# Kernel tuning notes

Hardware: AMD Instinct MI355X
Metric: run time of the kernel (lower is better)

## Reference

```python
import jax, jax.numpy as jnp
import numpy as np

B, N, L, VALID_Y = 1, 3072, 256, 200
DIM_X, DIM_Y, H = 3072, 1536, 24
HD = DIM_X // H  # 128
EPS_MOD, EPS_RMS = 1e-6, 1e-5


def _mod_rmsnorm(t, scale):
    # F.rms_norm (no weight) then modulate by (1 + scale)
    tn = t * jax.lax.rsqrt(jnp.mean(t * t, axis=-1, keepdims=True) + EPS_MOD)
    return tn * (1.0 + scale[:, None, :])


def _rmsnorm(t, w):
    return t * jax.lax.rsqrt(jnp.mean(t * t, axis=-1, keepdims=True) + EPS_RMS) * w


def _rope(t, cos, sin):
    # t: (B, N, H, HD); cos/sin: (N, H, HD/2); even/odd interleaved rotary
    te, to = t[..., 0::2], t[..., 1::2]
    cp = te * cos - to * sin
    sp = te * sin + to * cos
    return jnp.stack([cp, sp], axis=-1).reshape(t.shape)


def setup_inputs() -> dict:
    key = jax.random.key(0)
    ks = jax.random.split(key, 12)
    s = 0.02
    d = {}
    d['x'] = jax.random.normal(ks[0], (B, N, DIM_X), jnp.float32)
    d['y'] = jax.random.normal(ks[1], (B, L, DIM_Y), jnp.float32)
    d['scale_x'] = jax.random.normal(ks[2], (B, DIM_X), jnp.float32) * 0.1
    d['scale_y'] = jax.random.normal(ks[3], (B, DIM_Y), jnp.float32) * 0.1
    ang = jax.random.uniform(ks[4], (N, H, HD // 2), jnp.float32, 0.0, 2.0 * np.pi)
    d['rope_cos'] = jnp.cos(ang)
    d['rope_sin'] = jnp.sin(ang)
    d['W_qkv_x'] = jax.random.normal(ks[5], (DIM_X, 3 * DIM_X), jnp.float32) * s
    d['b_qkv_x'] = jnp.zeros((3 * DIM_X,), jnp.float32)
    d['W_qkv_y'] = jax.random.normal(ks[6], (DIM_Y, 3 * DIM_X), jnp.float32) * s
    d['b_qkv_y'] = jnp.zeros((3 * DIM_X,), jnp.float32)
    d['w_qn_x'] = jnp.ones((HD,), jnp.float32)
    d['w_kn_x'] = jnp.ones((HD,), jnp.float32)
    d['w_qn_y'] = jnp.ones((HD,), jnp.float32)
    d['w_kn_y'] = jnp.ones((HD,), jnp.float32)
    d['W_proj_x'] = jax.random.normal(ks[7], (DIM_X, DIM_X), jnp.float32) * s
    d['b_proj_x'] = jnp.zeros((DIM_X,), jnp.float32)
    d['W_proj_y'] = jax.random.normal(ks[8], (DIM_X, DIM_Y), jnp.float32) * s
    d['b_proj_y'] = jnp.zeros((DIM_Y,), jnp.float32)
    # B=1 packing: all N video tokens + first VALID_Y text tokens of flattened (N+L)
    d['valid_token_indices'] = jnp.arange(N + VALID_Y, dtype=jnp.int32)
    return d


def reference(x, y, scale_x, scale_y, rope_cos, rope_sin,
              W_qkv_x, b_qkv_x, W_qkv_y, b_qkv_y,
              w_qn_x, w_kn_x, w_qn_y, w_kn_y,
              W_proj_x, b_proj_x, W_proj_y, b_proj_y,
              valid_token_indices):
    # ---- visual stream: modulated RMSNorm -> qkv -> qk-norm -> RoPE ----
    xm = _mod_rmsnorm(x, scale_x)
    qkv_x = (xm @ W_qkv_x + b_qkv_x).reshape(B, N, 3, H, HD)
    qkv_x = jnp.transpose(qkv_x, (2, 0, 1, 3, 4))  # (3,B,N,H,HD)
    q_x, k_x, v_x = qkv_x[0], qkv_x[1], qkv_x[2]
    q_x = _rope(_rmsnorm(q_x, w_qn_x), rope_cos, rope_sin)
    k_x = _rope(_rmsnorm(k_x, w_kn_x), rope_cos, rope_sin)
    # ---- text stream: modulated RMSNorm -> qkv -> qk-norm ----
    ym = _mod_rmsnorm(y, scale_y)
    qkv_y = (ym @ W_qkv_y + b_qkv_y).reshape(B, L, 3, H, HD)
    q_y, k_y, v_y = qkv_y[:, :, 0], qkv_y[:, :, 1], qkv_y[:, :, 2]
    q_y = _rmsnorm(q_y, w_qn_y)
    k_y = _rmsnorm(k_y, w_kn_y)
    # ---- unify_streams: concat, pack, gather valid tokens ----
    qkv = jnp.stack([
        jnp.concatenate([q_x, q_y], axis=1),
        jnp.concatenate([k_x, k_y], axis=1),
        jnp.concatenate([v_x, v_y], axis=1),
    ], axis=2).reshape(B * (N + L), 3, H, HD)
    qkv = qkv[valid_token_indices]  # (total, 3, H, HD)
    q, k, v = qkv[:, 0], qkv[:, 1], qkv[:, 2]
    # ---- varlen attention (B=1 -> single segment, full attention) ----
    scale = 1.0 / np.sqrt(HD)
    scores = jnp.einsum('qhd,khd->hqk', q, k) * scale
    attn = jax.nn.softmax(scores, axis=-1)
    out = jnp.einsum('hqk,khd->qhd', attn, v).reshape(-1, H * HD)  # (total, DIM_X)
    # ---- pad_and_split_xy: scatter back to padded stream, split ----
    padded = jnp.zeros((B * (N + L), H * HD), out.dtype).at[valid_token_indices].set(out)
    padded = padded.reshape(B, N + L, H * HD)
    x_out = padded[:, :N] @ W_proj_x + b_proj_x
    y_out = padded[:, N:] @ W_proj_y + b_proj_y
    return (x_out, y_out)
```

## Files before the change

kernel.cpp:

```cpp
#include <hip/hip_runtime.h>


typedef short short8 __attribute__((ext_vector_type(8)));
typedef float f32x4 __attribute__((ext_vector_type(4)));
typedef unsigned short ushort4v __attribute__((ext_vector_type(4)));

#define MFMA_BF16(a,b,c) __builtin_amdgcn_mfma_f32_16x16x32_bf16((a),(b),(c),0,0,0)

#define NH 24
#define SPAD 3328
#define SVAL 3272

__device__ __forceinline__ unsigned short bf16_rne(float f){
  unsigned int u = __builtin_bit_cast(unsigned int, f);
  u += 0x7FFFu + ((u >> 16) & 1u);
  return (unsigned short)(u >> 16);
}
__device__ __forceinline__ float bf2f(unsigned short h){
  unsigned int u = ((unsigned int)h) << 16;
  return __builtin_bit_cast(float, u);
}
__device__ __forceinline__ void gload16(const void* g, void* l){
  __builtin_amdgcn_global_load_lds(
      (const __attribute__((address_space(1))) unsigned int*)g,
      (__attribute__((address_space(3))) unsigned int*)l, 16, 0, 0);
}

__global__ __launch_bounds__(256) void transpose_w(
    const float* __restrict__ W, unsigned short* __restrict__ Wt, int K, int N)
{
  __shared__ unsigned short t[64][66];
  int n0 = blockIdx.x*64, k0 = blockIdx.y*64;
  int tid = threadIdx.x;
  int kr = tid >> 4, nc = (tid & 15) * 4;
  #pragma unroll
  for (int pass=0; pass<4; pass++){
    int k = kr + pass*16;
    float4 v = *(const float4*)(W + (size_t)(k0+k)*N + n0 + nc);
    ushort4v o;
    o.x = bf16_rne(v.x); o.y = bf16_rne(v.y);
    o.z = bf16_rne(v.z); o.w = bf16_rne(v.w);
    *(ushort4v*)&t[k][nc] = o;
  }
  __syncthreads();
  int nr = tid >> 3, kc = (tid & 7) * 8;
  #pragma unroll
  for (int pass=0; pass<2; pass++){
    int n = nr + pass*32;
    unsigned short buf[8];
    #pragma unroll
    for (int j=0;j<8;j++) buf[j] = t[kc+j][n];
    *(short8*)(Wt + (size_t)(n0+n)*K + k0 + kc) = *(short8*)&buf[0];
  }
}

template<int D>
__global__ __launch_bounds__(256) void modnorm(
    const float* __restrict__ X, const float* __restrict__ scale,
    unsigned short* __restrict__ out)
{
  int row = blockIdx.x;
  const float4* xv = (const float4*)(X + (size_t)row*D);
  float ss = 0.f;
  for (int i = threadIdx.x; i < D/4; i += 256){
    float4 v = xv[i];
    ss += v.x*v.x + v.y*v.y + v.z*v.z + v.w*v.w;
  }
  #pragma unroll
  for (int d=1; d<64; d<<=1) ss += __shfl_xor(ss, d);
  __shared__ float wsum[4];
  if ((threadIdx.x & 63) == 0) wsum[threadIdx.x >> 6] = ss;
  __syncthreads();
  float tot = wsum[0] + wsum[1] + wsum[2] + wsum[3];
  float rn = rsqrtf(tot*(1.0f/(float)D) + 1e-6f);
  const float4* sv = (const float4*)scale;
  for (int i = threadIdx.x; i < D/4; i += 256){
    float4 v = xv[i]; float4 s4 = sv[i];
    ushort4v o;
    o.x = bf16_rne(v.x*rn*(1.f+s4.x));
    o.y = bf16_rne(v.y*rn*(1.f+s4.y));
    o.z = bf16_rne(v.z*rn*(1.f+s4.z));
    o.w = bf16_rne(v.w*rn*(1.f+s4.w));
    *(ushort4v*)(out + (size_t)row*D + i*4) = o;
  }
}

template<typename CT, bool BIAS>
__global__ __launch_bounds__(256, 3) void gemm_bt(
    const unsigned short* __restrict__ A, const unsigned short* __restrict__ BT,
    const float* __restrict__ bias, CT* __restrict__ C,
    int M, int N, int K, int ldc, int klen)
{
  __shared__ unsigned short lA[128*32];
  __shared__ unsigned short lB[128*32];
  int tid = threadIdx.x, wave = tid>>6, lane = tid&63;
  int l16 = lane&15, g = lane>>4;
  int wr = wave>>1, wc = wave&1;

  int nwg = gridDim.x*gridDim.y;
  int orig = blockIdx.y*gridDim.x + blockIdx.x;
  int neo = orig;
  if ((nwg & 7) == 0){
    int q8 = nwg >> 3;
    neo = (orig & 7)*q8 + (orig >> 3);
  }
  int bx = neo / gridDim.y;
  int by = neo % gridDim.y;
  int bm = by*128, bn = bx*128;
  int kof = blockIdx.z * klen;
  CT* Cp = C + (size_t)blockIdx.z * M * (size_t)ldc;

  f32x4 acc[4][4] = {};

  for (int k0 = kof; k0 < kof + klen; k0 += 32){
    #pragma unroll
    for (int i=0;i<2;i++){
      int off = i*4096 + wave*1024 + lane*16;
      int row = off>>6;
      int sp  = (off>>4)&3;
      int sk  = (sp ^ (row&3))*8;
      gload16(A + (size_t)(bm+row)*K + k0 + sk, (char*)lA + i*4096 + wave*1024);
    }
    #pragma unroll
    for (int i=0;i<2;i++){
      int off = i*4096 + wave*1024 + lane*16;
      int row = off>>6;
      int sp  = (off>>4)&3;
      int sk  = (sp ^ (row&3))*8;
      gload16(BT + (size_t)(bn+row)*K + k0 + sk, (char*)lB + i*4096 + wave*1024);
    }
    __syncthreads();

    short8 a[4], b[4];
    #pragma unroll
    for (int m=0;m<4;m++){
      int row = wr*64 + m*16 + l16;
      int slot = g ^ (row&3);
      a[m] = *(const short8*)((const char*)lA + row*64 + slot*16);
    }
    #pragma unroll
    for (int n=0;n<4;n++){
      int row = wc*64 + n*16 + l16;
      int slot = g ^ (row&3);
      b[n] = *(const short8*)((const char*)lB + row*64 + slot*16);
    }
    __builtin_amdgcn_s_setprio(1);
    #pragma unroll
    for (int m=0;m<4;m++)
      #pragma unroll
      for (int n=0;n<4;n++)
        acc[m][n] = MFMA_BF16(a[m], b[n], acc[m][n]);
    __builtin_amdgcn_s_setprio(0);
    __syncthreads();
  }

  #pragma unroll
  for (int n=0;n<4;n++){
    int col = bn + wc*64 + n*16 + l16;
    float bv = BIAS ? bias[col] : 0.f;
    #pragma unroll
    for (int m=0;m<4;m++){
      int row0 = bm + wr*64 + m*16 + g*4;
      #pragma unroll
      for (int r=0;r<4;r++){
        float v = acc[m][n][r] + bv;
        if constexpr (sizeof(CT) == 4) Cp[(size_t)(row0+r)*ldc + col] = v;
        else                           Cp[(size_t)(row0+r)*ldc + col] = bf16_rne(v);
      }
    }
  }
}

__global__ __launch_bounds__(512, 2) void gemm_8ph(
    const unsigned short* __restrict__ A, const unsigned short* __restrict__ BT,
    const float* __restrict__ bias, unsigned short* __restrict__ C,
    int M, int N, int K, int ldc)
{
  __shared__ unsigned short lds[8][8192];

  int tid = threadIdx.x, wave = tid>>6, lane = tid&63;
  int l16 = lane&15, g = lane>>4;
  int wr = wave>>2, wc = wave&3;

  int nwg = gridDim.x*gridDim.y;
  int orig = blockIdx.y*gridDim.x + blockIdx.x;
  int neo = orig;
  if ((nwg & 7) == 0) neo = (orig & 7)*(nwg>>3) + (orig>>3);
  int bx = neo / gridDim.y, by = neo % gridDim.y;
  int bm = by*256, bn = bx*256;

  const int NT = K >> 6;

  auto STAGE = [&](int t, int op, int half, int b){
    int tc = t < NT ? t : NT-1;
    const unsigned short* src = op ? BT : A;
    int base_row = (op ? bn : bm) + half*128;
    int k0 = tc << 6;
    #pragma unroll
    for (int j=0;j<2;j++){
      int o = (j*8 + wave)*1024 + lane*16;
      int row = o>>7, slot = (o>>4)&7;
      int sk = (slot ^ (row&7))*8;
      gload16(src + (size_t)(base_row+row)*K + k0 + sk,
              (char*)&lds[(b<<2)|(op<<1)|half][0] + (j*8+wave)*1024);
    }
  };

  short8 afr[4], bfr[8];
  auto LDA = [&](int b, int p){
    const char* basep = (const char*)&lds[(b<<2)|wr][0];
    #pragma unroll
    for (int mm=0;mm<2;mm++){
      int row = (p*2+mm)*16 + l16;
      #pragma unroll
      for (int kk=0;kk<2;kk++)
        afr[mm*2+kk] = *(const short8*)(basep + row*128 + (((kk*4+g) ^ (row&7))<<4));
    }
  };
  auto LDB = [&](int b){
    const char* basep = (const char*)&lds[(b<<2)|2|(wc>>1)][0];
    int rbase = (wc&1)*64;
    #pragma unroll
    for (int n=0;n<4;n++){
      int row = rbase + n*16 + l16;
      #pragma unroll
      for (int kk=0;kk<2;kk++)
        bfr[n*2+kk] = *(const short8*)(basep + row*128 + (((kk*4+g) ^ (row&7))<<4));
    }
  };

  f32x4 acc[8][4] = {};

  STAGE(0,1,0,0); STAGE(0,1,1,0); STAGE(0,0,0,0); STAGE(0,0,1,0);
  STAGE(1,1,0,1); STAGE(1,1,1,1); STAGE(1,0,0,1);
  asm volatile("s_waitcnt vmcnt(6)" ::: "memory");
  __builtin_amdgcn_s_barrier();

  int NIT = NT >> 1;
  for (int i=0;i<NIT;i++){
    int T = 2*i;
    #pragma unroll
    for (int p=0;p<4;p++){
      if (p==0) LDB(0);
      LDA(0, p);
      if (p==0)      STAGE(T+1,0,1,1);
      else if (p==1) STAGE(T+2,1,0,0);
      else if (p==2) STAGE(T+2,1,1,0);
      else           STAGE(T+2,0,0,0);
      if (p==0) asm volatile("s_waitcnt lgkmcnt(8)" ::: "memory");
      __builtin_amdgcn_s_barrier();
      asm volatile("s_waitcnt lgkmcnt(0)" ::: "memory");
      __builtin_amdgcn_sched_barrier(0);
      __builtin_amdgcn_s_setprio(1);
      #pragma unroll
      for (int mm=0;mm<2;mm++)
        #pragma unroll
        for (int n=0;n<4;n++)
          #pragma unroll
          for (int kk=0;kk<2;kk++)
            acc[p*2+mm][n] = MFMA_BF16(afr[mm*2+kk], bfr[n*2+kk], acc[p*2+mm][n]);
      __builtin_amdgcn_s_setprio(0);
      if (p==3) asm volatile("s_waitcnt vmcnt(6)" ::: "memory");
      __builtin_amdgcn_s_barrier();
    }
    #pragma unroll
    for (int p=0;p<4;p++){
      if (p==0) LDB(1);
      LDA(1, p);
      if (p==0)      STAGE(T+2,0,1,0);
      else if (p==1) STAGE(T+3,1,0,1);
      else if (p==2) STAGE(T+3,1,1,1);
      else           STAGE(T+3,0,0,1);
      if (p==0) asm volatile("s_waitcnt lgkmcnt(8)" ::: "memory");
      __builtin_amdgcn_s_barrier();
      asm volatile("s_waitcnt lgkmcnt(0)" ::: "memory");
      __builtin_amdgcn_sched_barrier(0);
      __builtin_amdgcn_s_setprio(1);
      #pragma unroll
      for (int mm=0;mm<2;mm++)
        #pragma unroll
        for (int n=0;n<4;n++)
          #pragma unroll
          for (int kk=0;kk<2;kk++)
            acc[p*2+mm][n] = MFMA_BF16(afr[mm*2+kk], bfr[n*2+kk], acc[p*2+mm][n]);
      __builtin_amdgcn_s_setprio(0);
      if (p==3) asm volatile("s_waitcnt vmcnt(6)" ::: "memory");
      __builtin_amdgcn_s_barrier();
    }
  }

  #pragma unroll
  for (int n=0;n<4;n++){
    int col = bn + wc*64 + n*16 + l16;
    float bv = bias[col];
    #pragma unroll
    for (int m=0;m<8;m++){
      int row0 = bm + wr*128 + m*16 + g*4;
      #pragma unroll
      for (int r=0;r<4;r++)
        C[(size_t)(row0+r)*ldc + col] = bf16_rne(acc[m][n][r] + bv);
    }
  }
}

__global__ __launch_bounds__(256) void reduce2_bias_bf16(
    const float* __restrict__ part, const float* __restrict__ bias,
    unsigned short* __restrict__ out, int N, size_t tot)
{
  size_t idx = ((size_t)blockIdx.x*256 + threadIdx.x)*4;
  if (idx >= tot) return;
  float4 a = *(const float4*)(part + idx);
  float4 b = *(const float4*)(part + tot + idx);
  int col = (int)(idx % N);
  float4 bv = *(const float4*)(bias + col);
  ushort4v o;
  o.x = bf16_rne(a.x+b.x+bv.x);
  o.y = bf16_rne(a.y+b.y+bv.y);
  o.z = bf16_rne(a.z+b.z+bv.z);
  o.w = bf16_rne(a.w+b.w+bv.w);
  *(ushort4v*)(out + idx) = o;
}

__global__ __launch_bounds__(256) void reduce8_bias_f32(
    const float* __restrict__ part, const float* __restrict__ bias,
    float* __restrict__ out, int N, size_t tot)
{
  size_t idx = ((size_t)blockIdx.x*256 + threadIdx.x)*4;
  if (idx >= tot) return;
  int col = (int)(idx % N);
  float4 s = *(const float4*)(bias + col);
  #pragma unroll
  for (int c=0;c<8;c++){
    float4 a = *(const float4*)(part + (size_t)c*tot + idx);
    s.x += a.x; s.y += a.y; s.z += a.z; s.w += a.w;
  }
  *(float4*)(out + idx) = s;
}

__global__ __launch_bounds__(256) void fixup_qk(
    const unsigned short* __restrict__ QKV,
    const float* __restrict__ cosT, const float* __restrict__ sinT,
    const float* __restrict__ wqx, const float* __restrict__ wkx,
    const float* __restrict__ wqy, const float* __restrict__ wky,
    unsigned short* __restrict__ Qo, unsigned short* __restrict__ Ko)
{
  int wave = threadIdx.x >> 6, lane = threadIdx.x & 63;
  int bid = blockIdx.x*4 + wave;
  int t = bid / NH, h = bid % NH;
  bool isx = (t < 3072);

  const unsigned short* base = QKV + (size_t)t*9216 + h*128;
  unsigned int qraw = *(const unsigned int*)(base + 2*lane);
  unsigned int kraw = *(const unsigned int*)(base + 3072 + 2*lane);
  float q0 = bf2f((unsigned short)(qraw & 0xffff)), q1 = bf2f((unsigned short)(qraw >> 16));
  float k0 = bf2f((unsigned short)(kraw & 0xffff)), k1 = bf2f((unsigned short)(kraw >> 16));

  float sq = q0*q0 + q1*q1, sk = k0*k0 + k1*k1;
  #pragma unroll
  for (int d=1; d<64; d<<=1){ sq += __shfl_xor(sq, d); sk += __shfl_xor(sk, d); }
  float rq = rsqrtf(sq*(1.0f/128.0f) + 1e-5f);
  float rk = rsqrtf(sk*(1.0f/128.0f) + 1e-5f);

  const float* wq = isx ? wqx : wqy;
  const float* wk = isx ? wkx : wky;
  float a0 = q0*rq*wq[2*lane], a1 = q1*rq*wq[2*lane+1];
  float b0 = k0*rk*wk[2*lane], b1 = k1*rk*wk[2*lane+1];

  if (isx){
    size_t ci = ((size_t)t*NH + h)*64 + lane;
    float c = cosT[ci], s = sinT[ci];
    float t0 = a0*c - a1*s, t1 = a0*s + a1*c; a0 = t0; a1 = t1;
    t0 = b0*c - b1*s; t1 = b0*s + b1*c; b0 = t0; b1 = t1;
  }
  size_t oi = ((size_t)h*SPAD + t)*128 + 2*lane;
  *(unsigned int*)(Qo + oi) = (unsigned int)bf16_rne(a0) | ((unsigned int)bf16_rne(a1) << 16);
  *(unsigned int*)(Ko + oi) = (unsigned int)bf16_rne(b0) | ((unsigned int)bf16_rne(b1) << 16);
}

__global__ __launch_bounds__(256) void v_transpose(
    const unsigned short* __restrict__ QKV, unsigned short* __restrict__ VT)
{
  __shared__ unsigned short t[64][136];
  int h = blockIdx.x;
  int t0 = blockIdx.y*64;
  int tid = threadIdx.x;
  #pragma unroll
  for (int it=0; it<4; it++){
    int chunk = it*256 + tid;
    int r = chunk >> 4, c = chunk & 15;
    short8 v = *(const short8*)(QKV + (size_t)(t0 + r)*9216 + 6144 + h*128 + c*8);
    *(short8*)&t[r][c*8] = v;
  }
  __syncthreads();
  int d = tid >> 1, half = tid & 1;
  size_t ob = (size_t)(h*128 + d)*SPAD + t0 + half*32;
  #pragma unroll
  for (int j=0;j<32;j+=2){
    unsigned int v = (unsigned int)t[half*32 + j][d] | ((unsigned int)t[half*32 + j + 1][d] << 16);
    *(unsigned int*)(VT + ob + j) = v;
  }
}

__global__ __launch_bounds__(256, 3) void attn_fwd(
    const unsigned short* __restrict__ Q, const unsigned short* __restrict__ Kb,
    const unsigned short* __restrict__ VT, unsigned short* __restrict__ O)
{
  __shared__ unsigned short lK[2][32*128];
  __shared__ unsigned short lV[2][128*32];
  __shared__ unsigned short lP[4][32*72];

  int tid = threadIdx.x, wave = tid>>6, lane = tid&63;
  int l16 = lane&15, g = lane>>4;
  int h = blockIdx.x, qt = blockIdx.y;
  int q0 = qt*128 + wave*32;

  auto STAGE = [&](int kt, int b){
    #pragma unroll
    for (int i=0;i<2;i++){
      int off = (i*4 + wave)*1024 + lane*16;
      int row = off>>8;
      int sp  = (off>>4)&15;
      int ssp = sp ^ (row&7);
      gload16(Kb + ((size_t)h*SPAD + kt*32 + row)*128 + ssp*8,
              (char*)&lK[b][0] + (i*4 + wave)*1024);
    }
    #pragma unroll
    for (int i=0;i<2;i++){
      int off = (i*4 + wave)*1024 + lane*16;
      int row = off>>6;
      int sp  = (off>>4)&3;
      int ssp = sp ^ ((row>>1)&3);
      gload16(VT + ((size_t)(h*128 + row))*SPAD + kt*32 + ssp*8,
              (char*)&lV[b][0] + (i*4 + wave)*1024);
    }
  };

  short8 qf[2][4];
  const unsigned short* qbase = Q + (size_t)h*SPAD*128;
  #pragma unroll
  for (int mt=0;mt<2;mt++){
    int row = q0 + mt*16 + l16;
    #pragma unroll
    for (int ks=0;ks<4;ks++)
      qf[mt][ks] = *(const short8*)(qbase + (size_t)row*128 + ks*32 + g*8);
  }

  f32x4 oacc[2][8] = {};
  float lsum[2][4] = {};

  unsigned short* lPw = &lP[wave][0];
  const float sc2 = 0.08838834764831845f * 1.4426950408889634f;
  const float C2  = -12.0f * 1.4426950408889634f;

  STAGE(0, 0);

  for (int kt=0; kt<104; kt++){
    int cur = kt & 1;
    int nxt = (kt+1 < 104) ? kt+1 : 103;
    STAGE(nxt, cur ^ 1);
    asm volatile("s_waitcnt vmcnt(4)" ::: "memory");
    __builtin_amdgcn_s_barrier();

    const char* lKc = (const char*)&lK[cur][0];
    const char* lVc = (const char*)&lV[cur][0];

    f32x4 s[2][2] = {};
    #pragma unroll
    for (int ks=0;ks<4;ks++){
      short8 bfrag[2];
      #pragma unroll
      for (int nt=0;nt<2;nt++){
        int row = nt*16 + l16;
        int slot = (ks*4 + g) ^ (row&7);
        bfrag[nt] = *(const short8*)(lKc + row*256 + slot*16);
      }
      __builtin_amdgcn_s_setprio(1);
      #pragma unroll
      for (int mt=0;mt<2;mt++)
        #pragma unroll
        for (int nt=0;nt<2;nt++)
          s[mt][nt] = MFMA_BF16(qf[mt][ks], bfrag[nt], s[mt][nt]);
      __builtin_amdgcn_s_setprio(0);
    }

    bool edge = (kt >= 102);
    #pragma unroll
    for (int mt=0;mt<2;mt++)
      #pragma unroll
      for (int nt=0;nt<2;nt++){
        #pragma unroll
        for (int r=0;r<4;r++){
          float p = __builtin_amdgcn_exp2f(fmaf(s[mt][nt][r], sc2, C2));
          if (edge){
            int key = kt*32 + nt*16 + l16;
            if (key >= SVAL) p = 0.f;
          }
          lsum[mt][r] += p;
          lPw[(mt*16 + g*4 + r)*72 + nt*16 + l16] = bf16_rne(p);
        }
      }

    asm volatile("s_waitcnt lgkmcnt(0)" ::: "memory");

    {
      short8 pa[2];
      #pragma unroll
      for (int mt=0;mt<2;mt++)
        pa[mt] = *(const short8*)(lPw + (mt*16 + l16)*72 + g*8);
      __builtin_amdgcn_s_setprio(1);
      #pragma unroll
      for (int dt=0;dt<8;dt++){
        int row = dt*16 + l16;
        int slot = g ^ ((row>>1)&3);
        short8 vb = *(const short8*)(lVc + row*64 + slot*16);
        #pragma unroll
        for (int mt=0;mt<2;mt++)
          oacc[mt][dt] = MFMA_BF16(pa[mt], vb, oacc[mt][dt]);
      }
      __builtin_amdgcn_s_setprio(0);
    }
    __builtin_amdgcn_s_barrier();
  }

  #pragma unroll
  for (int mt=0;mt<2;mt++){
    float inv[4];
    #pragma unroll
    for (int r=0;r<4;r++){
      float v = lsum[mt][r];
      v += __shfl_xor(v, 1); v += __shfl_xor(v, 2);
      v += __shfl_xor(v, 4); v += __shfl_xor(v, 8);
      inv[r] = 1.0f / v;
    }
    #pragma unroll
    for (int dt=0;dt<8;dt++)
      #pragma unroll
      for (int r=0;r<4;r++){
        int row = q0 + mt*16 + g*4 + r;
        if (row < SVAL)
          O[(size_t)row*3072 + h*128 + dt*16 + l16] = bf16_rne(oacc[mt][dt][r]*inv[r]);
      }
  }
}

static const size_t OFF_WT_QKV_X  = 0;
static const size_t OFF_WT_QKV_Y  = 56623104;
static const size_t OFF_WT_PROJ_X = 84934656;
static const size_t OFF_WT_PROJ_Y = 103809024;
static const size_t OFF_XM        = 113246208;
static const size_t OFF_YM        = 132120576;
static const size_t OFF_QKV       = 132907008;
static const size_t OFF_Q         = 194248704;
static const size_t OFF_K         = 214695936;
static const size_t OFF_VT        = 235143168;
static const size_t WS_NEEDED     = 255590400;
static const size_t OFF_AO        = 0;

extern "C" void kernel_launch(void* const* d_in, const int* in_sizes, int n_in,
                              void* d_out, int out_size, void* d_ws, size_t ws_size,
                              hipStream_t stream) {
  if (ws_size < WS_NEEDED) return;

  const float* x        = (const float*)d_in[0];
  const float* y        = (const float*)d_in[1];
  const float* scale_x  = (const float*)d_in[2];
  const float* scale_y  = (const float*)d_in[3];
  const float* rope_cos = (const float*)d_in[4];
  const float* rope_sin = (const float*)d_in[5];
  const float* W_qkv_x  = (const float*)d_in[6];
  const float* b_qkv_x  = (const float*)d_in[7];
  const float* W_qkv_y  = (const float*)d_in[8];
  const float* b_qkv_y  = (const float*)d_in[9];
  const float* w_qn_x   = (const float*)d_in[10];
  const float* w_kn_x   = (const float*)d_in[11];
  const float* w_qn_y   = (const float*)d_in[12];
  const float* w_kn_y   = (const float*)d_in[13];
  const float* W_proj_x = (const float*)d_in[14];
  const float* b_proj_x = (const float*)d_in[15];
  const float* W_proj_y = (const float*)d_in[16];
  const float* b_proj_y = (const float*)d_in[17];

  float* out_x = (float*)d_out;
  float* out_y = out_x + (size_t)3072*3072;

  char* ws = (char*)d_ws;
  unsigned short* Wt_qkv_x  = (unsigned short*)(ws + OFF_WT_QKV_X);
  unsigned short* Wt_qkv_y  = (unsigned short*)(ws + OFF_WT_QKV_Y);
  unsigned short* Wt_proj_x = (unsigned short*)(ws + OFF_WT_PROJ_X);
  unsigned short* Wt_proj_y = (unsigned short*)(ws + OFF_WT_PROJ_Y);
  unsigned short* xm        = (unsigned short*)(ws + OFF_XM);
  unsigned short* ym        = (unsigned short*)(ws + OFF_YM);
  unsigned short* qkv       = (unsigned short*)(ws + OFF_QKV);
  unsigned short* Qb        = (unsigned short*)(ws + OFF_Q);
  unsigned short* Kb        = (unsigned short*)(ws + OFF_K);
  unsigned short* VTb       = (unsigned short*)(ws + OFF_VT);
  unsigned short* attnout   = (unsigned short*)(ws + OFF_AO);
  float* part_qkv_y         = (float*)(ws + OFF_XM);
  float* part_proj_y        = (float*)(ws + OFF_Q);

  transpose_w<<<dim3(9216/64, 3072/64), 256, 0, stream>>>(W_qkv_x,  Wt_qkv_x,  3072, 9216);
  transpose_w<<<dim3(9216/64, 1536/64), 256, 0, stream>>>(W_qkv_y,  Wt_qkv_y,  1536, 9216);
  transpose_w<<<dim3(3072/64, 3072/64), 256, 0, stream>>>(W_proj_x, Wt_proj_x, 3072, 3072);
  transpose_w<<<dim3(1536/64, 3072/64), 256, 0, stream>>>(W_proj_y, Wt_proj_y, 3072, 1536);

  modnorm<3072><<<3072, 256, 0, stream>>>(x, scale_x, xm);
  modnorm<1536><<<256,  256, 0, stream>>>(y, scale_y, ym);

  gemm_8ph<<<dim3(36, 12), 512, 0, stream>>>(
      xm, Wt_qkv_x, b_qkv_x, qkv, 3072, 9216, 3072, 9216);

  gemm_bt<float, false><<<dim3(72, 2, 2), 256, 0, stream>>>(
      ym, Wt_qkv_y, nullptr, part_qkv_y, 256, 9216, 1536, 9216, 768);
  reduce2_bias_bf16<<<2304, 256, 0, stream>>>(
      part_qkv_y, b_qkv_y, qkv + (size_t)3072*9216, 9216, (size_t)256*9216);

  fixup_qk<<<SVAL*NH/4, 256, 0, stream>>>(qkv, rope_cos, rope_sin,
                                          w_qn_x, w_kn_x, w_qn_y, w_kn_y, Qb, Kb);
  v_transpose<<<dim3(NH, SPAD/64), 256, 0, stream>>>(qkv, VTb);

  (void)hipMemsetAsync(attnout + (size_t)SVAL*3072, 0,
                       (size_t)(SPAD - SVAL)*3072*2, stream);

  attn_fwd<<<dim3(NH, SPAD/128), 256, 0, stream>>>(Qb, Kb, VTb, attnout);

  gemm_bt<float, true><<<dim3(24, 24, 1), 256, 0, stream>>>(
      attnout, Wt_proj_x, b_proj_x, out_x, 3072, 3072, 3072, 3072, 3072);

  gemm_bt<float, false><<<dim3(12, 2, 8), 256, 0, stream>>>(
      attnout + (size_t)3072*3072, Wt_proj_y, nullptr, part_proj_y,
      256, 1536, 3072, 1536, 384);
  reduce8_bias_f32<<<384, 256, 0, stream>>>(
      part_proj_y, b_proj_y, out_y, 1536, (size_t)256*1536);
}
```

Before: 602.8 us.

## Fold y-stream GEMMs into x-stream launches as an extra tile row

The y-stream QKV GEMM is merged into the x-stream QKV GEMM launch as an extra row of 256x256 tiles (grid 36x13). The y-stream projection GEMM is merged into the x-stream projection launch as an extra row of 128x128 tiles (grid 24x25). This removes the split-K partial buffers, two reduction kernels and separate launches. The XCD swizzle is generalised to grid sizes that are not multiples of 8. In exchange, the y tiles run full K without split-K, so the extra tile row may finish later than the rest of the grid and lengthen the tail.

```diff
diff --git a/kernel.cpp b/kernel.cpp
--- a/kernel.cpp
+++ b/kernel.cpp
@@ -24,6 +24,11 @@
   __builtin_amdgcn_global_load_lds(
       (const __attribute__((address_space(1))) unsigned int*)g,
       (__attribute__((address_space(3))) unsigned int*)l, 16, 0, 0);
+}
+__device__ __forceinline__ int xcd_swizzle(int orig, int nwg){
+  int q = nwg >> 3, r = nwg & 7;
+  int xcd = orig & 7, loc = orig >> 3;
+  return (xcd < r ? xcd*(q+1) : r*(q+1) + (xcd-r)*q) + loc;
 }
 
 __global__ __launch_bounds__(256) void transpose_w(
@@ -85,96 +90,12 @@
   }
 }
 
-template<typename CT, bool BIAS>
-__global__ __launch_bounds__(256, 3) void gemm_bt(
-    const unsigned short* __restrict__ A, const unsigned short* __restrict__ BT,
-    const float* __restrict__ bias, CT* __restrict__ C,
-    int M, int N, int K, int ldc, int klen)
-{
-  __shared__ unsigned short lA[128*32];
-  __shared__ unsigned short lB[128*32];
-  int tid = threadIdx.x, wave = tid>>6, lane = tid&63;
-  int l16 = lane&15, g = lane>>4;
-  int wr = wave>>1, wc = wave&1;
-
-  int nwg = gridDim.x*gridDim.y;
-  int orig = blockIdx.y*gridDim.x + blockIdx.x;
-  int neo = orig;
-  if ((nwg & 7) == 0){
-    int q8 = nwg >> 3;
-    neo = (orig & 7)*q8 + (orig >> 3);
-  }
-  int bx = neo / gridDim.y;
-  int by = neo % gridDim.y;
-  int bm = by*128, bn = bx*128;
-  int kof = blockIdx.z * klen;
-  CT* Cp = C + (size_t)blockIdx.z * M * (size_t)ldc;
-
-  f32x4 acc[4][4] = {};
-
-  for (int k0 = kof; k0 < kof + klen; k0 += 32){
-    #pragma unroll
-    for (int i=0;i<2;i++){
-      int off = i*4096 + wave*1024 + lane*16;
-      int row = off>>6;
-      int sp  = (off>>4)&3;
-      int sk  = (sp ^ (row&3))*8;
-      gload16(A + (size_t)(bm+row)*K + k0 + sk, (char*)lA + i*4096 + wave*1024);
-    }
-    #pragma unroll
-    for (int i=0;i<2;i++){
-      int off = i*4096 + wave*1024 + lane*16;
-      int row = off>>6;
-      int sp  = (off>>4)&3;
-      int sk  = (sp ^ (row&3))*8;
-      gload16(BT + (size_t)(bn+row)*K + k0 + sk, (char*)lB + i*4096 + wave*1024);
-    }
-    __syncthreads();
-
-    short8 a[4], b[4];
-    #pragma unroll
-    for (int m=0;m<4;m++){
-      int row = wr*64 + m*16 + l16;
-      int slot = g ^ (row&3);
-      a[m] = *(const short8*)((const char*)lA + row*64 + slot*16);
-    }
-    #pragma unroll
-    for (int n=0;n<4;n++){
-      int row = wc*64 + n*16 + l16;
-      int slot = g ^ (row&3);
-      b[n] = *(const short8*)((const char*)lB + row*64 + slot*16);
-    }
-    __builtin_amdgcn_s_setprio(1);
-    #pragma unroll
-    for (int m=0;m<4;m++)
-      #pragma unroll
-      for (int n=0;n<4;n++)
-        acc[m][n] = MFMA_BF16(a[m], b[n], acc[m][n]);
-    __builtin_amdgcn_s_setprio(0);
-    __syncthreads();
-  }
-
-  #pragma unroll
-  for (int n=0;n<4;n++){
-    int col = bn + wc*64 + n*16 + l16;
-    float bv = BIAS ? bias[col] : 0.f;
-    #pragma unroll
-    for (int m=0;m<4;m++){
-      int row0 = bm + wr*64 + m*16 + g*4;
-      #pragma unroll
-      for (int r=0;r<4;r++){
-        float v = acc[m][n][r] + bv;
-        if constexpr (sizeof(CT) == 4) Cp[(size_t)(row0+r)*ldc + col] = v;
-        else                           Cp[(size_t)(row0+r)*ldc + col] = bf16_rne(v);
-      }
-    }
-  }
-}
-
 __global__ __launch_bounds__(512, 2) void gemm_8ph(
     const unsigned short* __restrict__ A, const unsigned short* __restrict__ BT,
     const float* __restrict__ bias, unsigned short* __restrict__ C,
-    int M, int N, int K, int ldc)
+    int K, int ldc,
+    const unsigned short* __restrict__ A2, const unsigned short* __restrict__ BT2,
+    const float* __restrict__ bias2, unsigned short* __restrict__ C2, int K2)
 {
   __shared__ unsigned short lds[8][8192];
 
@@ -184,16 +105,23 @@
 
   int nwg = gridDim.x*gridDim.y;
   int orig = blockIdx.y*gridDim.x + blockIdx.x;
-  int neo = orig;
-  if ((nwg & 7) == 0) neo = (orig & 7)*(nwg>>3) + (orig>>3);
+  int neo = xcd_swizzle(orig, nwg);
   int bx = neo / gridDim.y, by = neo % gridDim.y;
-  int bm = by*256, bn = bx*256;
-
-  const int NT = K >> 6;
+
+  bool ybl = (by == (int)gridDim.y - 1);
+  const unsigned short* Ap  = ybl ? A2 : A;
+  const unsigned short* Bp  = ybl ? BT2 : BT;
+  const float* bp           = ybl ? bias2 : bias;
+  unsigned short* Cp        = ybl ? C2 : C;
+  int Kl = ybl ? K2 : K;
+  int bm = ybl ? 0 : by*256;
+  int bn = bx*256;
+
+  const int NT = Kl >> 6;
 
   auto STAGE = [&](int t, int op, int half, int b){
     int tc = t < NT ? t : NT-1;
-    const unsigned short* src = op ? BT : A;
+    const unsigned short* src = op ? Bp : Ap;
     int base_row = (op ? bn : bm) + half*128;
     int k0 = tc << 6;
     #pragma unroll
@@ -201,7 +129,7 @@
       int o = (j*8 + wave)*1024 + lane*16;
       int row = o>>7, slot = (o>>4)&7;
       int sk = (slot ^ (row&7))*8;
-      gload16(src + (size_t)(base_row+row)*K + k0 + sk,
+      gload16(src + (size_t)(base_row+row)*Kl + k0 + sk,
               (char*)&lds[(b<<2)|(op<<1)|half][0] + (j*8+wave)*1024);
     }
   };
@@ -292,49 +220,101 @@
   #pragma unroll
   for (int n=0;n<4;n++){
     int col = bn + wc*64 + n*16 + l16;
-    float bv = bias[col];
+    float bv = bp[col];
     #pragma unroll
     for (int m=0;m<8;m++){
       int row0 = bm + wr*128 + m*16 + g*4;
       #pragma unroll
       for (int r=0;r<4;r++)
-        C[(size_t)(row0+r)*ldc + col] = bf16_rne(acc[m][n][r] + bv);
-    }
-  }
-}
-
-__global__ __launch_bounds__(256) void reduce2_bias_bf16(
-    const float* __restrict__ part, const float* __restrict__ bias,
-    unsigned short* __restrict__ out, int N, size_t tot)
+        Cp[(size_t)(row0+r)*ldc + col] = bf16_rne(acc[m][n][r] + bv);
+    }
+  }
+}
+
+__global__ __launch_bounds__(256, 3) void gemm_proj(
+    const unsigned short* __restrict__ A, const unsigned short* __restrict__ BT,
+    const float* __restrict__ bias, float* __restrict__ C, int ldc,
+    const unsigned short* __restrict__ A2, const unsigned short* __restrict__ BT2,
+    const float* __restrict__ bias2, float* __restrict__ C2, int ldc2)
 {
-  size_t idx = ((size_t)blockIdx.x*256 + threadIdx.x)*4;
-  if (idx >= tot) return;
-  float4 a = *(const float4*)(part + idx);
-  float4 b = *(const float4*)(part + tot + idx);
-  int col = (int)(idx % N);
-  float4 bv = *(const float4*)(bias + col);
-  ushort4v o;
-  o.x = bf16_rne(a.x+b.x+bv.x);
-  o.y = bf16_rne(a.y+b.y+bv.y);
-  o.z = bf16_rne(a.z+b.z+bv.z);
-  o.w = bf16_rne(a.w+b.w+bv.w);
-  *(ushort4v*)(out + idx) = o;
-}
-
-__global__ __launch_bounds__(256) void reduce8_bias_f32(
-    const float* __restrict__ part, const float* __restrict__ bias,
-    float* __restrict__ out, int N, size_t tot)
-{
-  size_t idx = ((size_t)blockIdx.x*256 + threadIdx.x)*4;
-  if (idx >= tot) return;
-  int col = (int)(idx % N);
-  float4 s = *(const float4*)(bias + col);
-  #pragma unroll
-  for (int c=0;c<8;c++){
-    float4 a = *(const float4*)(part + (size_t)c*tot + idx);
-    s.x += a.x; s.y += a.y; s.z += a.z; s.w += a.w;
-  }
-  *(float4*)(out + idx) = s;
+  __shared__ unsigned short lA[128*32];
+  __shared__ unsigned short lB[128*32];
+  int tid = threadIdx.x, wave = tid>>6, lane = tid&63;
+  int l16 = lane&15, g = lane>>4;
+  int wr = wave>>1, wc = wave&1;
+
+  const int K = 3072;
+  int nwg = gridDim.x*gridDim.y;
+  int orig = blockIdx.y*gridDim.x + blockIdx.x;
+  int neo = xcd_swizzle(orig, nwg);
+  int bx = neo / gridDim.y, by = neo % gridDim.y;
+
+  bool ybl = (by == (int)gridDim.y - 1);
+  const unsigned short* Ap = ybl ? A2 : A;
+  const unsigned short* Bp = ybl ? BT2 : BT;
+  const float* bp          = ybl ? bias2 : bias;
+  float* Cp                = ybl ? C2 : C;
+  int ldcl                 = ybl ? ldc2 : ldc;
+  int bm, bn;
+  if (ybl){ bm = (bx & 1)*128; bn = (bx >> 1)*128; }
+  else    { bm = by*128;       bn = bx*128; }
+
+  f32x4 acc[4][4] = {};
+
+  for (int k0 = 0; k0 < K; k0 += 32){
+    #pragma unroll
+    for (int i=0;i<2;i++){
+      int off = i*4096 + wave*1024 + lane*16;
+      int row = off>>6;
+      int sp  = (off>>4)&3;
+      int sk  = (sp ^ (row&3))*8;
+      gload16(Ap + (size_t)(bm+row)*K + k0 + sk, (char*)lA + i*4096 + wave*1024);
+    }
+    #pragma unroll
+    for (int i=0;i<2;i++){
+      int off = i*4096 + wave*1024 + lane*16;
+      int row = off>>6;
+      int sp  = (off>>4)&3;
+      int sk  = (sp ^ (row&3))*8;
+      gload16(Bp + (size_t)(bn+row)*K + k0 + sk, (char*)lB + i*4096 + wave*1024);
+    }
+    __syncthreads();
+
+    short8 a[4], b[4];
+    #pragma unroll
+    for (int m=0;m<4;m++){
+      int row = wr*64 + m*16 + l16;
+      int slot = g ^ (row&3);
+      a[m] = *(const short8*)((const char*)lA + row*64 + slot*16);
+    }
+    #pragma unroll
+    for (int n=0;n<4;n++){
+      int row = wc*64 + n*16 + l16;
+      int slot = g ^ (row&3);
+      b[n] = *(const short8*)((const char*)lB + row*64 + slot*16);
+    }
+    __builtin_amdgcn_s_setprio(1);
+    #pragma unroll
+    for (int m=0;m<4;m++)
+      #pragma unroll
+      for (int n=0;n<4;n++)
+        acc[m][n] = MFMA_BF16(a[m], b[n], acc[m][n]);
+    __builtin_amdgcn_s_setprio(0);
+    __syncthreads();
+  }
+
+  #pragma unroll
+  for (int n=0;n<4;n++){
+    int col = bn + wc*64 + n*16 + l16;
+    float bv = bp[col];
+    #pragma unroll
+    for (int m=0;m<4;m++){
+      int row0 = bm + wr*64 + m*16 + g*4;
+      #pragma unroll
+      for (int r=0;r<4;r++)
+        Cp[(size_t)(row0+r)*ldcl + col] = acc[m][n][r] + bv;
+    }
+  }
 }
 
 __global__ __launch_bounds__(256) void fixup_qk(
@@ -595,8 +575,6 @@
   unsigned short* Kb        = (unsigned short*)(ws + OFF_K);
   unsigned short* VTb       = (unsigned short*)(ws + OFF_VT);
   unsigned short* attnout   = (unsigned short*)(ws + OFF_AO);
-  float* part_qkv_y         = (float*)(ws + OFF_XM);
-  float* part_proj_y        = (float*)(ws + OFF_Q);
 
   transpose_w<<<dim3(9216/64, 3072/64), 256, 0, stream>>>(W_qkv_x,  Wt_qkv_x,  3072, 9216);
   transpose_w<<<dim3(9216/64, 1536/64), 256, 0, stream>>>(W_qkv_y,  Wt_qkv_y,  1536, 9216);
@@ -606,13 +584,9 @@
   modnorm<3072><<<3072, 256, 0, stream>>>(x, scale_x, xm);
   modnorm<1536><<<256,  256, 0, stream>>>(y, scale_y, ym);
 
-  gemm_8ph<<<dim3(36, 12), 512, 0, stream>>>(
-      xm, Wt_qkv_x, b_qkv_x, qkv, 3072, 9216, 3072, 9216);
-
-  gemm_bt<float, false><<<dim3(72, 2, 2), 256, 0, stream>>>(
-      ym, Wt_qkv_y, nullptr, part_qkv_y, 256, 9216, 1536, 9216, 768);
-  reduce2_bias_bf16<<<2304, 256, 0, stream>>>(
-      part_qkv_y, b_qkv_y, qkv + (size_t)3072*9216, 9216, (size_t)256*9216);
+  gemm_8ph<<<dim3(36, 13), 512, 0, stream>>>(
+      xm, Wt_qkv_x, b_qkv_x, qkv, 3072, 9216,
+      ym, Wt_qkv_y, b_qkv_y, qkv + (size_t)3072*9216, 1536);
 
   fixup_qk<<<SVAL*NH/4, 256, 0, stream>>>(qkv, rope_cos, rope_sin,
                                           w_qn_x, w_kn_x, w_qn_y, w_kn_y, Qb, Kb);
@@ -623,12 +597,7 @@
 
   attn_fwd<<<dim3(NH, SPAD/128), 256, 0, stream>>>(Qb, Kb, VTb, attnout);
 
-  gemm_bt<float, true><<<dim3(24, 24, 1), 256, 0, stream>>>(
-      attnout, Wt_proj_x, b_proj_x, out_x, 3072, 3072, 3072, 3072, 3072);
-
-  gemm_bt<float, false><<<dim3(12, 2, 8), 256, 0, stream>>>(
-      attnout + (size_t)3072*3072, Wt_proj_y, nullptr, part_proj_y,
-      256, 1536, 3072, 1536, 384);
-  reduce8_bias_f32<<<384, 256, 0, stream>>>(
-      part_proj_y, b_proj_y, out_y, 1536, (size_t)256*1536);
-}
+  gemm_proj<<<dim3(24, 25), 256, 0, stream>>>(
+      attnout, Wt_proj_x, b_proj_x, out_x, 3072,
+      attnout + (size_t)3072*3072, Wt_proj_y, b_proj_y, out_y, 1536);
+}
```

Result: faster. 551.9 us (-8.4%).
